# Optimization experiments

Hardware: AMD Instinct MI355X
Metric: run time of the kernel (lower is better)

Reference implementation:

```python
import jax, jax.numpy as jnp
import numpy as np

EPS = 1e-5
NEG_SLOPE = 0.01  # torch F.leaky_relu default


def _batchnorm(h, gamma, beta):
    # BatchNorm1d in training mode: batch stats over node dim, biased variance
    mu = jnp.mean(h, axis=0)
    var = jnp.mean((h - mu) ** 2, axis=0)
    return gamma * (h - mu) * jax.lax.rsqrt(var + EPS) + beta


def setup_inputs() -> dict:
    N, E, H, ED = 16384, 524288, 128, 16
    key = jax.random.key(0)
    ks = jax.random.split(key, 12)
    s = 1.0 / np.sqrt(H)
    return {
        "x": jax.random.normal(ks[0], (N, H), jnp.float32),
        "edge_index": jax.random.randint(ks[1], (2, E), 0, N, jnp.int64),
        "edge_attr": jax.random.normal(ks[2], (E, ED), jnp.float32),
        "Wq": jax.random.normal(ks[3], (H, H), jnp.float32) * s,
        "bq": jnp.zeros((H,), jnp.float32),
        "Wk": jax.random.normal(ks[4], (H, H), jnp.float32) * s,
        "bk": jnp.zeros((H,), jnp.float32),
        "Wv": jax.random.normal(ks[5], (H, H), jnp.float32) * s,
        "bv": jnp.zeros((H,), jnp.float32),
        "We": jax.random.normal(ks[6], (ED, 1), jnp.float32) * (1.0 / np.sqrt(ED)),
        "be": jnp.zeros((1,), jnp.float32),
        "bn1_g": jnp.ones((H,), jnp.float32),
        "bn1_b": jnp.zeros((H,), jnp.float32),
        "W1": jax.random.normal(ks[7], (H, 2 * H), jnp.float32) * s,
        "b1": jnp.zeros((2 * H,), jnp.float32),
        "W2": jax.random.normal(ks[8], (2 * H, H), jnp.float32) * (1.0 / np.sqrt(2 * H)),
        "b2": jnp.zeros((H,), jnp.float32),
        "bn2_g": jnp.ones((H,), jnp.float32),
        "bn2_b": jnp.zeros((H,), jnp.float32),
    }


def reference(x, edge_index, edge_attr, Wq, bq, Wk, bk, Wv, bv, We, be,
              bn1_g, bn1_b, W1, b1, W2, b2, bn2_g, bn2_b):
    N = x.shape[0]
    Q = x @ Wq + bq  # [N, H]
    K = x @ Wk + bk
    V = x @ Wv + bv
    Ebias = (edge_attr @ We + be)[:, 0]  # [E], num_heads == 1
    src, dst = edge_index[0], edge_index[1]
    # per-edge dot product over the FULL hidden dim (as in the source)
    scores = jnp.sum(Q[src] * K[dst], axis=1) + Ebias  # [E]
    scores = jnp.where(scores >= 0, scores, NEG_SLOPE * scores)
    # to_dense_adj scatter-adds edge_attr into a dense [N, N] adjacency
    adj = jnp.zeros((N, N), x.dtype).at[src, dst].add(scores)
    attn = jax.nn.softmax(adj, axis=1)  # dense softmax incl. zero non-edges
    x_new = attn @ V  # [N, H]
    h = _batchnorm(x + x_new, bn1_g, bn1_b)
    ffn = jax.nn.relu(h @ W1 + b1) @ W2 + b2
    return _batchnorm(h + ffn, bn2_g, bn2_b)
```

## Files before the change

kernel.cpp:

```cpp
#include <hip/hip_runtime.h>
#include <hip/hip_bf16.h>
#include <math.h>

#define H 128
#define H2 256
#define SLAB 96
#define LDA 136
#define LDA2 264

typedef __attribute__((ext_vector_type(8))) short s16x8;
typedef __attribute__((ext_vector_type(4))) float f32x4;

__device__ __forceinline__ unsigned short f2bf(float f) {
  unsigned u = __float_as_uint(f);
  unsigned r = (u + 0x7FFFu + ((u >> 16) & 1u)) >> 16;
  return (unsigned short)r;
}
__device__ __forceinline__ float bf2f(unsigned short s) {
  return __uint_as_float(((unsigned)s) << 16);
}

__global__ void wprep(const float* __restrict__ Wq, const float* __restrict__ Wk,
                      const float* __restrict__ Wv, const float* __restrict__ W1,
                      const float* __restrict__ W2,
                      short* qh, short* ql, short* kh, short* kl,
                      short* vh, short* w1h, short* w2h)
{
  int job = blockIdx.z;
  const float* src; short* dh; short* dl = nullptr; int Kd, Nn;
  if (job == 0)      { src = Wq; dh = qh;  dl = ql; Kd = 128; Nn = 128; }
  else if (job == 1) { src = Wk; dh = kh;  dl = kl; Kd = 128; Nn = 128; }
  else if (job == 2) { src = Wv; dh = vh;           Kd = 128; Nn = 128; }
  else if (job == 3) { src = W1; dh = w1h;          Kd = 128; Nn = 256; }
  else               { src = W2; dh = w2h;          Kd = 256; Nn = 128; }
  int t = blockIdx.x * 256 + threadIdx.x;
  if (t >= Kd * Nn) return;
  int n = t / Kd, k = t - n * Kd;
  float v = src[(size_t)k * Nn + n];
  unsigned short h = f2bf(v);
  dh[t] = (short)h;
  if (dl) dl[t] = (short)f2bf(v - bf2f(h));
}

__global__ __launch_bounds__(256) void qkv_mfma(
    const float* __restrict__ x,
    const short* __restrict__ Wqh, const short* __restrict__ Wql,
    const short* __restrict__ Wkh, const short* __restrict__ Wkl,
    const short* __restrict__ Wvh,
    const float* __restrict__ bq, const float* __restrict__ bk,
    const float* __restrict__ bv,
    float* __restrict__ Q, unsigned short* __restrict__ Kbf,
    unsigned short* __restrict__ Vbf, float* __restrict__ SV)
{
  __shared__ __align__(16) short Ahi[64 * LDA];
  __shared__ __align__(16) short Alo[64 * LDA];
  __shared__ __align__(16) short Bhi[128 * LDA];
  __shared__ __align__(16) short Blo[128 * LDA];
  int tid = threadIdx.x;
  int bm = blockIdx.x * 64;
  int wave = tid >> 6, lane = tid & 63;
  int quad = lane >> 4, l16 = lane & 15;
  int wn = wave * 32;

#pragma unroll
  for (int i = 0; i < 4; ++i) {
    int g = i * 256 + tid;
    int row = g >> 4, f = g & 15;
    const float4* xp = (const float4*)&x[(size_t)(bm + row) * H + f * 8];
    float4 v0 = xp[0], v1 = xp[1];
    float vv[8] = {v0.x, v0.y, v0.z, v0.w, v1.x, v1.y, v1.z, v1.w};
    s16x8 hv, lv;
#pragma unroll
    for (int j = 0; j < 8; ++j) {
      unsigned short hh = f2bf(vv[j]);
      hv[j] = (short)hh;
      lv[j] = (short)f2bf(vv[j] - bf2f(hh));
    }
    *(s16x8*)&Ahi[row * LDA + f * 8] = hv;
    *(s16x8*)&Alo[row * LDA + f * 8] = lv;
  }

  for (int ph = 0; ph < 3; ++ph) {
    const short* Bh = (ph == 0) ? Wqh : (ph == 1) ? Wkh : Wvh;
    const short* Bl = (ph == 0) ? Wql : (ph == 1) ? Wkl : nullptr;
    if (ph > 0) __syncthreads();
#pragma unroll
    for (int i = 0; i < 8; ++i) {
      int g = i * 256 + tid;
      int n = g >> 4, f = g & 15;
      *(s16x8*)&Bhi[n * LDA + f * 8] = *(const s16x8*)&Bh[n * H + f * 8];
      if (Bl) *(s16x8*)&Blo[n * LDA + f * 8] = *(const s16x8*)&Bl[n * H + f * 8];
    }
    __syncthreads();

    f32x4 acc[4][2];
#pragma unroll
    for (int mt = 0; mt < 4; ++mt)
#pragma unroll
      for (int nt = 0; nt < 2; ++nt) acc[mt][nt] = (f32x4){0.f, 0.f, 0.f, 0.f};

#pragma unroll
    for (int ks = 0; ks < 4; ++ks) {
      int kof = ks * 32 + quad * 8;
      s16x8 ah[4], al[4], bh[2], bl2[2];
#pragma unroll
      for (int mt = 0; mt < 4; ++mt) {
        ah[mt] = *(s16x8*)&Ahi[(mt * 16 + l16) * LDA + kof];
        al[mt] = *(s16x8*)&Alo[(mt * 16 + l16) * LDA + kof];
      }
#pragma unroll
      for (int nt = 0; nt < 2; ++nt) {
        bh[nt] = *(s16x8*)&Bhi[(wn + nt * 16 + l16) * LDA + kof];
        bl2[nt] = *(s16x8*)&Blo[(wn + nt * 16 + l16) * LDA + kof];
      }
#pragma unroll
      for (int mt = 0; mt < 4; ++mt)
#pragma unroll
        for (int nt = 0; nt < 2; ++nt) {
          acc[mt][nt] = __builtin_amdgcn_mfma_f32_16x16x32_bf16(ah[mt], bh[nt], acc[mt][nt], 0, 0, 0);
          if (ph < 2) {
            acc[mt][nt] = __builtin_amdgcn_mfma_f32_16x16x32_bf16(ah[mt], bl2[nt], acc[mt][nt], 0, 0, 0);
            acc[mt][nt] = __builtin_amdgcn_mfma_f32_16x16x32_bf16(al[mt], bh[nt], acc[mt][nt], 0, 0, 0);
          }
        }
    }

    if (ph == 0) {
#pragma unroll
      for (int nt = 0; nt < 2; ++nt) {
        int col = wn + nt * 16 + l16;
        float bb = bq[col];
#pragma unroll
        for (int mt = 0; mt < 4; ++mt)
#pragma unroll
          for (int r = 0; r < 4; ++r) {
            int row = bm + mt * 16 + quad * 4 + r;
            Q[(size_t)row * H + col] = acc[mt][nt][r] + bb;
          }
      }
    } else if (ph == 1) {
#pragma unroll
      for (int nt = 0; nt < 2; ++nt) {
        int col = wn + nt * 16 + l16;
        float bb = bk[col];
#pragma unroll
        for (int mt = 0; mt < 4; ++mt)
#pragma unroll
          for (int r = 0; r < 4; ++r) {
            int row = bm + mt * 16 + quad * 4 + r;
            Kbf[(size_t)row * H + col] = f2bf(acc[mt][nt][r] + bb);
          }
      }
    } else {
#pragma unroll
      for (int nt = 0; nt < 2; ++nt) {
        int col = wn + nt * 16 + l16;
        float bb = bv[col];
        float ps = 0.f;
#pragma unroll
        for (int mt = 0; mt < 4; ++mt)
#pragma unroll
          for (int r = 0; r < 4; ++r) {
            int row = bm + mt * 16 + quad * 4 + r;
            float v = acc[mt][nt][r] + bb;
            Vbf[(size_t)row * H + col] = f2bf(v);
            ps += v;
          }
        ps += __shfl_xor(ps, 16);
        ps += __shfl_xor(ps, 32);
        if (quad == 0) atomicAdd(&SV[col], ps);
      }
    }
  }
}

__global__ __launch_bounds__(256) void ffn1_mfma(
    const float* __restrict__ h1, const short* __restrict__ W1h,
    const float* __restrict__ b1, const float* __restrict__ A1,
    const float* __restrict__ B1, unsigned short* __restrict__ t1)
{
  __shared__ __align__(16) short As[64 * LDA];
  __shared__ __align__(16) short Bs[256 * LDA];
  int tid = threadIdx.x;
  int bm = blockIdx.x * 64;
  int wave = tid >> 6, lane = tid & 63;
  int quad = lane >> 4, l16 = lane & 15;
  int wn = wave * 64;

#pragma unroll
  for (int i = 0; i < 4; ++i) {
    int g = i * 256 + tid;
    int row = g >> 4, f = g & 15;
    const float4* xp = (const float4*)&h1[(size_t)(bm + row) * H + f * 8];
    float4 v0 = xp[0], v1 = xp[1];
    const float4* ap = (const float4*)&A1[f * 8];
    const float4* bp = (const float4*)&B1[f * 8];
    float4 a0 = ap[0], a1 = ap[1], b0 = bp[0], b1v = bp[1];
    float vv[8] = {a0.x * v0.x + b0.x, a0.y * v0.y + b0.y,
                   a0.z * v0.z + b0.z, a0.w * v0.w + b0.w,
                   a1.x * v1.x + b1v.x, a1.y * v1.y + b1v.y,
                   a1.z * v1.z + b1v.z, a1.w * v1.w + b1v.w};
    s16x8 hv;
#pragma unroll
    for (int j = 0; j < 8; ++j) hv[j] = (short)f2bf(vv[j]);
    *(s16x8*)&As[row * LDA + f * 8] = hv;
  }
#pragma unroll
  for (int i = 0; i < 16; ++i) {
    int g = i * 256 + tid;
    int n = g >> 4, f = g & 15;
    *(s16x8*)&Bs[n * LDA + f * 8] = *(const s16x8*)&W1h[n * H + f * 8];
  }
  __syncthreads();

  f32x4 acc[4][4];
#pragma unroll
  for (int mt = 0; mt < 4; ++mt)
#pragma unroll
    for (int nt = 0; nt < 4; ++nt) acc[mt][nt] = (f32x4){0.f, 0.f, 0.f, 0.f};

#pragma unroll
  for (int ks = 0; ks < 4; ++ks) {
    int kof = ks * 32 + quad * 8;
    s16x8 ah[4], bh[4];
#pragma unroll
    for (int mt = 0; mt < 4; ++mt) ah[mt] = *(s16x8*)&As[(mt * 16 + l16) * LDA + kof];
#pragma unroll
    for (int nt = 0; nt < 4; ++nt) bh[nt] = *(s16x8*)&Bs[(wn + nt * 16 + l16) * LDA + kof];
#pragma unroll
    for (int mt = 0; mt < 4; ++mt)
#pragma unroll
      for (int nt = 0; nt < 4; ++nt)
        acc[mt][nt] = __builtin_amdgcn_mfma_f32_16x16x32_bf16(ah[mt], bh[nt], acc[mt][nt], 0, 0, 0);
  }

#pragma unroll
  for (int nt = 0; nt < 4; ++nt) {
    int col = wn + nt * 16 + l16;
    float bb = b1[col];
#pragma unroll
    for (int mt = 0; mt < 4; ++mt)
#pragma unroll
      for (int r = 0; r < 4; ++r) {
        int row = bm + mt * 16 + quad * 4 + r;
        float v = acc[mt][nt][r] + bb;
        v = v > 0.f ? v : 0.f;
        t1[(size_t)row * H2 + col] = f2bf(v);
      }
  }
}

__global__ __launch_bounds__(256) void ffn2_mfma(
    const unsigned short* __restrict__ t1, const short* __restrict__ W2h,
    const float* __restrict__ b2, const float* __restrict__ h1,
    const float* __restrict__ A1, const float* __restrict__ B1,
    float* __restrict__ h2, float* __restrict__ sum2, float* __restrict__ sq2)
{
  __shared__ __align__(16) short As[64 * LDA2];
  __shared__ __align__(16) short Bs[128 * LDA2];
  int tid = threadIdx.x;
  int bm = blockIdx.x * 64;
  int wave = tid >> 6, lane = tid & 63;
  int quad = lane >> 4, l16 = lane & 15;
  int wn = wave * 32;

#pragma unroll
  for (int i = 0; i < 8; ++i) {
    int g = i * 256 + tid;
    int row = g >> 5, f = g & 31;
    *(s16x8*)&As[row * LDA2 + f * 8] = *(const s16x8*)&t1[(size_t)(bm + row) * H2 + f * 8];
  }
#pragma unroll
  for (int i = 0; i < 16; ++i) {
    int g = i * 256 + tid;
    int n = g >> 5, f = g & 31;
    *(s16x8*)&Bs[n * LDA2 + f * 8] = *(const s16x8*)&W2h[n * H2 + f * 8];
  }
  __syncthreads();

  f32x4 acc[4][2];
#pragma unroll
  for (int mt = 0; mt < 4; ++mt)
#pragma unroll
    for (int nt = 0; nt < 2; ++nt) acc[mt][nt] = (f32x4){0.f, 0.f, 0.f, 0.f};

#pragma unroll
  for (int ks = 0; ks < 8; ++ks) {
    int kof = ks * 32 + quad * 8;
    s16x8 ah[4], bh[2];
#pragma unroll
    for (int mt = 0; mt < 4; ++mt) ah[mt] = *(s16x8*)&As[(mt * 16 + l16) * LDA2 + kof];
#pragma unroll
    for (int nt = 0; nt < 2; ++nt) bh[nt] = *(s16x8*)&Bs[(wn + nt * 16 + l16) * LDA2 + kof];
#pragma unroll
    for (int mt = 0; mt < 4; ++mt)
#pragma unroll
      for (int nt = 0; nt < 2; ++nt)
        acc[mt][nt] = __builtin_amdgcn_mfma_f32_16x16x32_bf16(ah[mt], bh[nt], acc[mt][nt], 0, 0, 0);
  }

#pragma unroll
  for (int nt = 0; nt < 2; ++nt) {
    int col = wn + nt * 16 + l16;
    float bb = b2[col], ra = A1[col], rb = B1[col];
    float ps = 0.f, pq = 0.f;
#pragma unroll
    for (int mt = 0; mt < 4; ++mt)
#pragma unroll
      for (int r = 0; r < 4; ++r) {
        int row = bm + mt * 16 + quad * 4 + r;
        float rr = ra * h1[(size_t)row * H + col] + rb;
        float v = acc[mt][nt][r] + bb + rr;
        h2[(size_t)row * H + col] = v;
        ps += v; pq += v * v;
      }
    ps += __shfl_xor(ps, 16); ps += __shfl_xor(ps, 32);
    pq += __shfl_xor(pq, 16); pq += __shfl_xor(pq, 32);
    if (quad == 0) {
      atomicAdd(&sum2[col], ps);
      atomicAdd(&sq2[col], pq);
    }
  }
}

__global__ void ebfill(const float* __restrict__ ea,
                       const float* __restrict__ We,
                       const float* __restrict__ be,
                       const int* __restrict__ ei,
                       int* __restrict__ cnt,
                       int2* __restrict__ slabDE, int E, int N)
{
  int grp = blockIdx.x & 7;
  int blk = blockIdx.x >> 3;
  int lo = grp * (N >> 3), hi = lo + (N >> 3);
  int per = E >> 8;
  int base = blk * per;
  float4 w0 = *(const float4*)&We[0], w1 = *(const float4*)&We[4];
  float4 w2 = *(const float4*)&We[8], w3 = *(const float4*)&We[12];
  float bias = be[0];
  for (int i = 0; i < per; i += 256) {
    int e = base + i + threadIdx.x;
    if (e >= E) continue;
    int src = ei[e];
    if (src < lo || src >= hi) continue;
    int dst = ei[E + e];
    const float4* p = (const float4*)&ea[(size_t)e * 16];
    float4 a0 = p[0], a1 = p[1], a2 = p[2], a3 = p[3];
    float s = a0.x * w0.x + a0.y * w0.y + a0.z * w0.z + a0.w * w0.w
            + a1.x * w1.x + a1.y * w1.y + a1.z * w1.z + a1.w * w1.w
            + a2.x * w2.x + a2.y * w2.y + a2.z * w2.z + a2.w * w2.w
            + a3.x * w3.x + a3.y * w3.y + a3.z * w3.z + a3.w * w3.w;
    s += bias;
    int pos = atomicAdd(&cnt[src], 1);
    if (pos < SLAB) {
      int2 rec; rec.x = dst; rec.y = __float_as_int(s);
      slabDE[src * SLAB + pos] = rec;
    }
  }
}

__global__ __launch_bounds__(256) void score_slab(
    const float* __restrict__ Q, const unsigned short* __restrict__ Kbf,
    const int* __restrict__ cnt, const int2* __restrict__ slabDE,
    float* __restrict__ sAslab, int N)
{
  int tid = threadIdx.x;
  int team = tid >> 3, sub = tid & 7;
  int local = team & 15;
  int i = blockIdx.x * 2 + (team >> 4);
  int k = cnt[i]; if (k > SLAB) k = SLAB;
  const float4* q4 = (const float4*)(Q + (size_t)i * H);
  float4 qa0 = q4[2 * sub], qa1 = q4[2 * sub + 1];
  float4 qb0 = q4[16 + 2 * sub], qb1 = q4[17 + 2 * sub];
  int base = i * SLAB;

  for (int p = local * 2; p < k; p += 32) {
    int2 de0 = slabDE[base + p];
    bool has1 = (p + 1 < k);
    int2 de1 = has1 ? slabDE[base + p + 1] : de0;
    const s16x8* k0 = (const s16x8*)(Kbf + (size_t)de0.x * H);
    const s16x8* k1 = (const s16x8*)(Kbf + (size_t)de1.x * H);
    s16x8 ka0 = k0[sub], kb0 = k0[8 + sub];
    s16x8 ka1 = k1[sub], kb1 = k1[8 + sub];
    float p0, p1;
    p0 = qa0.x * bf2f((unsigned short)ka0[0]) + qa0.y * bf2f((unsigned short)ka0[1])
       + qa0.z * bf2f((unsigned short)ka0[2]) + qa0.w * bf2f((unsigned short)ka0[3])
       + qa1.x * bf2f((unsigned short)ka0[4]) + qa1.y * bf2f((unsigned short)ka0[5])
       + qa1.z * bf2f((unsigned short)ka0[6]) + qa1.w * bf2f((unsigned short)ka0[7])
       + qb0.x * bf2f((unsigned short)kb0[0]) + qb0.y * bf2f((unsigned short)kb0[1])
       + qb0.z * bf2f((unsigned short)kb0[2]) + qb0.w * bf2f((unsigned short)kb0[3])
       + qb1.x * bf2f((unsigned short)kb0[4]) + qb1.y * bf2f((unsigned short)kb0[5])
       + qb1.z * bf2f((unsigned short)kb0[6]) + qb1.w * bf2f((unsigned short)kb0[7]);
    p1 = qa0.x * bf2f((unsigned short)ka1[0]) + qa0.y * bf2f((unsigned short)ka1[1])
       + qa0.z * bf2f((unsigned short)ka1[2]) + qa0.w * bf2f((unsigned short)ka1[3])
       + qa1.x * bf2f((unsigned short)ka1[4]) + qa1.y * bf2f((unsigned short)ka1[5])
       + qa1.z * bf2f((unsigned short)ka1[6]) + qa1.w * bf2f((unsigned short)ka1[7])
       + qb0.x * bf2f((unsigned short)kb1[0]) + qb0.y * bf2f((unsigned short)kb1[1])
       + qb0.z * bf2f((unsigned short)kb1[2]) + qb0.w * bf2f((unsigned short)kb1[3])
       + qb1.x * bf2f((unsigned short)kb1[4]) + qb1.y * bf2f((unsigned short)kb1[5])
       + qb1.z * bf2f((unsigned short)kb1[6]) + qb1.w * bf2f((unsigned short)kb1[7]);
    p0 += __shfl_xor(p0, 1); p1 += __shfl_xor(p1, 1);
    p0 += __shfl_xor(p0, 2); p1 += __shfl_xor(p1, 2);
    p0 += __shfl_xor(p0, 4); p1 += __shfl_xor(p1, 4);
    if (sub == 0) {
      float s0 = p0 + __int_as_float(de0.y);
      sAslab[base + p] = (s0 >= 0.f) ? s0 : 0.01f * s0;
      if (has1) {
        float s1 = p1 + __int_as_float(de1.y);
        sAslab[base + p + 1] = (s1 >= 0.f) ? s1 : 0.01f * s1;
      }
    }
  }
}

__global__ __launch_bounds__(256) void row_slab(
    const float* __restrict__ x, const unsigned short* __restrict__ Vbf,
    const float* __restrict__ SV, const int* __restrict__ cnt,
    const float* __restrict__ sAslab, const int2* __restrict__ slabDE,
    float* __restrict__ h1, int N)
{
  __shared__ float sv[8][SLAB];
  __shared__ int sd[8][SLAB];
  __shared__ unsigned char sown[8][SLAB];
  int team = threadIdx.x >> 5, lane = threadIdx.x & 31;
  int i = blockIdx.x * 8 + team;
  int k = cnt[i]; if (k > SLAB) k = SLAB;
  int base = i * SLAB;

  for (int p = lane; p < k; p += 32) {
    sv[team][p] = sAslab[base + p];
    sd[team][p] = slabDE[base + p].x;
  }
  __syncthreads();

  for (int p = lane; p < k; p += 32) {
    int d = sd[team][p], o = p;
    for (int q = 0; q < p; ++q)
      if (sd[team][q] == d) { o = q; break; }
    sown[team][p] = (unsigned char)o;
  }
  __syncthreads();
  for (int p = lane; p < k; p += 32)
    if (sown[team][p] != (unsigned char)p)
      atomicAdd(&sv[team][sown[team][p]], sv[team][p]);
  __syncthreads();

  float m = 0.f;
  for (int p = lane; p < k; p += 32)
    if (sown[team][p] == (unsigned char)p) m = fmaxf(m, sv[team][p]);
#pragma unroll
  for (int mask = 16; mask; mask >>= 1) m = fmaxf(m, __shfl_xor(m, mask));
  float em = expf(-m);

  float zl = 0.f;
  for (int p = lane; p < k; p += 32) {
    float cf = 0.f;
    if (sown[team][p] == (unsigned char)p) cf = expf(sv[team][p] - m) - em;
    sv[team][p] = cf;
    zl += cf;
  }
#pragma unroll
  for (int mask = 16; mask; mask >>= 1) zl += __shfl_xor(zl, mask);
  float Zi = 1.f / ((float)N * em + zl);
  __syncthreads();

  const ushort4* V4 = (const ushort4*)Vbf;
  float4 s4 = *(const float4*)&SV[lane * 4];
  float ax = em * s4.x, ay = em * s4.y, az = em * s4.z, aw = em * s4.w;
  int c = 0;
  for (; c + 8 <= k; c += 8) {
    float cf[8]; int dd[8]; ushort4 vv[8];
#pragma unroll
    for (int u = 0; u < 8; ++u) { cf[u] = sv[team][c + u]; dd[u] = sd[team][c + u]; }
#pragma unroll
    for (int u = 0; u < 8; ++u) vv[u] = V4[(size_t)dd[u] * 32 + lane];
#pragma unroll
    for (int u = 0; u < 8; ++u) {
      ax += cf[u] * bf2f(vv[u].x);
      ay += cf[u] * bf2f(vv[u].y);
      az += cf[u] * bf2f(vv[u].z);
      aw += cf[u] * bf2f(vv[u].w);
    }
  }
  for (; c < k; ++c) {
    float cf = sv[team][c];
    ushort4 v0 = V4[(size_t)sd[team][c] * 32 + lane];
    ax += cf * bf2f(v0.x); ay += cf * bf2f(v0.y);
    az += cf * bf2f(v0.z); aw += cf * bf2f(v0.w);
  }
  float4 xx = *(const float4*)&x[(size_t)i * H + lane * 4];
  float4 out;
  out.x = xx.x + ax * Zi; out.y = xx.y + ay * Zi;
  out.z = xx.z + az * Zi; out.w = xx.w + aw * Zi;
  *(float4*)&h1[(size_t)i * H + lane * 4] = out;
}

__global__ __launch_bounds__(128) void colstats(
    const float* __restrict__ X, float* __restrict__ sum,
    float* __restrict__ sumsq, int rowsPerBlock)
{
  int t = threadIdx.x;
  size_t r0 = (size_t)blockIdx.x * rowsPerBlock;
  float s = 0.f, ss = 0.f;
  for (int r = 0; r < rowsPerBlock; ++r) {
    float v = X[(r0 + r) * H + t];
    s += v; ss += v * v;
  }
  atomicAdd(&sum[t], s);
  atomicAdd(&sumsq[t], ss);
}

__global__ void bn_final(const float* __restrict__ sum, const float* __restrict__ sumsq,
                         const float* __restrict__ g, const float* __restrict__ b,
                         float* __restrict__ A, float* __restrict__ B, int n)
{
  int t = threadIdx.x;
  float mu = sum[t] / (float)n;
  float var = sumsq[t] / (float)n - mu * mu;
  float rs = rsqrtf(var + 1e-5f);
  float a = g[t] * rs;
  A[t] = a;
  B[t] = b[t] - a * mu;
}

__global__ void bn_apply(const float* __restrict__ X, const float* __restrict__ A,
                         const float* __restrict__ B, float* __restrict__ Y, size_t n4)
{
  size_t i = (size_t)blockIdx.x * blockDim.x + threadIdx.x;
  if (i >= n4) return;
  float4 v = ((const float4*)X)[i];
  int c = (int)((i * 4) & (H - 1));
  float4 a = *(const float4*)&A[c];
  float4 b = *(const float4*)&B[c];
  v.x = a.x * v.x + b.x; v.y = a.y * v.y + b.y;
  v.z = a.z * v.z + b.z; v.w = a.w * v.w + b.w;
  ((float4*)Y)[i] = v;
}

extern "C" void kernel_launch(void* const* d_in, const int* in_sizes, int n_in,
                              void* d_out, int out_size, void* d_ws, size_t ws_size,
                              hipStream_t stream)
{
  const float* x  = (const float*)d_in[0];
  const int*   ei = (const int*)d_in[1];
  const float* ea = (const float*)d_in[2];
  const float* Wq = (const float*)d_in[3];
  const float* bq = (const float*)d_in[4];
  const float* Wk = (const float*)d_in[5];
  const float* bk = (const float*)d_in[6];
  const float* Wv = (const float*)d_in[7];
  const float* bv = (const float*)d_in[8];
  const float* We = (const float*)d_in[9];
  const float* be = (const float*)d_in[10];
  const float* g1 = (const float*)d_in[11];
  const float* bb1 = (const float*)d_in[12];
  const float* W1 = (const float*)d_in[13];
  const float* b1 = (const float*)d_in[14];
  const float* W2 = (const float*)d_in[15];
  const float* b2 = (const float*)d_in[16];
  const float* g2 = (const float*)d_in[17];
  const float* bb2 = (const float*)d_in[18];

  int N = in_sizes[0] / H;
  int E = in_sizes[2] / 16;
  size_t NH = (size_t)N * H;

  float* Q   = (float*)d_ws;
  float* KmSlot = Q + NH;
  float* h1  = KmSlot + NH;
  unsigned short* Vbf = (unsigned short*)(h1 + NH);
  int2*  slabDE = (int2*)(Vbf + NH);
  float* sAslab = (float*)(slabDE + (size_t)N * SLAB);
  int*   cnt    = (int*)(sAslab + (size_t)N * SLAB);
  float* stats  = (float*)(cnt + N);
  float* SV   = stats;
  float* sum1 = stats + H;
  float* sq1  = stats + 2 * H;
  float* sum2 = stats + 3 * H;
  float* sq2  = stats + 4 * H;
  float* A1   = stats + 5 * H;
  float* B1   = stats + 6 * H;
  float* A2   = stats + 7 * H;
  float* B2   = stats + 8 * H;
  short* wbuf = (short*)(stats + 9 * H + 4);
  short* Wqh = wbuf;
  short* Wql = Wqh + 16384;
  short* Wkh = Wql + 16384;
  short* Wkl = Wkh + 16384;
  short* Wvh = Wkl + 16384;
  short* W1h = Wvh + 16384;
  short* W2h = W1h + 32768;
  unsigned short* Kbf = (unsigned short*)KmSlot;
  unsigned short* t1 = (unsigned short*)Q;
  float* h2 = KmSlot;

  hipMemsetAsync(cnt, 0, (size_t)N * sizeof(int), stream);
  hipMemsetAsync(stats, 0, (size_t)5 * H * sizeof(float), stream);

  wprep<<<dim3(128, 1, 5), 256, 0, stream>>>(Wq, Wk, Wv, W1, W2,
      Wqh, Wql, Wkh, Wkl, Wvh, W1h, W2h);

  qkv_mfma<<<dim3(N / 64), 256, 0, stream>>>(
      x, Wqh, Wql, Wkh, Wkl, Wvh, bq, bk, bv, Q, Kbf, Vbf, SV);

  ebfill<<<dim3(2048), 256, 0, stream>>>(ea, We, be, ei, cnt, slabDE, E, N);
  score_slab<<<dim3(N / 2), 256, 0, stream>>>(Q, Kbf, cnt, slabDE, sAslab, N);
  row_slab<<<dim3(N / 8), 256, 0, stream>>>(x, Vbf, SV, cnt, sAslab, slabDE, h1, N);

  colstats<<<dim3(128), 128, 0, stream>>>(h1, sum1, sq1, N / 128);
  bn_final<<<dim3(1), H, 0, stream>>>(sum1, sq1, g1, bb1, A1, B1, N);

  ffn1_mfma<<<dim3(N / 64), 256, 0, stream>>>(h1, W1h, b1, A1, B1, t1);
  ffn2_mfma<<<dim3(N / 64), 256, 0, stream>>>(t1, W2h, b2, h1, A1, B1, h2, sum2, sq2);

  bn_final<<<dim3(1), H, 0, stream>>>(sum2, sq2, g2, bb2, A2, B2, N);
  bn_apply<<<dim3((int)((NH / 4 + 255) / 256)), 256, 0, stream>>>(h2, A2, B2, (float*)d_out, NH / 4);
}
```

Measured before the change: 264.9 us.

## Load MFMA weight fragments directly into registers and fold BN finalize into consumers

The QKV, FFN1 and FFN2 GEMM kernels stop staging weight tiles in shared memory and instead load each wave's B fragments straight from global memory into registers. This removes large LDS allocations and the associated stores and barriers, which can raise occupancy. The two single-block bn_final launches are removed, and each consumer kernel recomputes the BatchNorm scale and shift from the sum and sum-of-squares buffers. The trade-off is more register pressure, redundant global weight reads per wave that now rely on cache hits, and repeated rsqrt work in every thread.

```diff
diff --git a/kernel.cpp b/kernel.cpp
--- a/kernel.cpp
+++ b/kernel.cpp
@@ -7,6 +7,7 @@
 #define SLAB 96
 #define LDA 136
 #define LDA2 264
+#define EPS 1e-5f
 
 typedef __attribute__((ext_vector_type(8))) short s16x8;
 typedef __attribute__((ext_vector_type(4))) float f32x4;
@@ -54,8 +55,6 @@
 {
   __shared__ __align__(16) short Ahi[64 * LDA];
   __shared__ __align__(16) short Alo[64 * LDA];
-  __shared__ __align__(16) short Bhi[128 * LDA];
-  __shared__ __align__(16) short Blo[128 * LDA];
   int tid = threadIdx.x;
   int bm = blockIdx.x * 64;
   int wave = tid >> 6, lane = tid & 63;
@@ -79,19 +78,25 @@
     *(s16x8*)&Ahi[row * LDA + f * 8] = hv;
     *(s16x8*)&Alo[row * LDA + f * 8] = lv;
   }
+  __syncthreads();
 
   for (int ph = 0; ph < 3; ++ph) {
     const short* Bh = (ph == 0) ? Wqh : (ph == 1) ? Wkh : Wvh;
     const short* Bl = (ph == 0) ? Wql : (ph == 1) ? Wkl : nullptr;
-    if (ph > 0) __syncthreads();
-#pragma unroll
-    for (int i = 0; i < 8; ++i) {
-      int g = i * 256 + tid;
-      int n = g >> 4, f = g & 15;
-      *(s16x8*)&Bhi[n * LDA + f * 8] = *(const s16x8*)&Bh[n * H + f * 8];
-      if (Bl) *(s16x8*)&Blo[n * LDA + f * 8] = *(const s16x8*)&Bl[n * H + f * 8];
-    }
-    __syncthreads();
+
+    s16x8 bh[2][4], bl2[2][4];
+#pragma unroll
+    for (int nt = 0; nt < 2; ++nt)
+#pragma unroll
+      for (int ks = 0; ks < 4; ++ks)
+        bh[nt][ks] = *(const s16x8*)&Bh[(size_t)(wn + nt * 16 + l16) * H + ks * 32 + quad * 8];
+    if (Bl) {
+#pragma unroll
+      for (int nt = 0; nt < 2; ++nt)
+#pragma unroll
+        for (int ks = 0; ks < 4; ++ks)
+          bl2[nt][ks] = *(const s16x8*)&Bl[(size_t)(wn + nt * 16 + l16) * H + ks * 32 + quad * 8];
+    }
 
     f32x4 acc[4][2];
 #pragma unroll
@@ -102,25 +107,20 @@
 #pragma unroll
     for (int ks = 0; ks < 4; ++ks) {
       int kof = ks * 32 + quad * 8;
-      s16x8 ah[4], al[4], bh[2], bl2[2];
+      s16x8 ah[4], al[4];
 #pragma unroll
       for (int mt = 0; mt < 4; ++mt) {
         ah[mt] = *(s16x8*)&Ahi[(mt * 16 + l16) * LDA + kof];
         al[mt] = *(s16x8*)&Alo[(mt * 16 + l16) * LDA + kof];
       }
 #pragma unroll
-      for (int nt = 0; nt < 2; ++nt) {
-        bh[nt] = *(s16x8*)&Bhi[(wn + nt * 16 + l16) * LDA + kof];
-        bl2[nt] = *(s16x8*)&Blo[(wn + nt * 16 + l16) * LDA + kof];
-      }
-#pragma unroll
       for (int mt = 0; mt < 4; ++mt)
 #pragma unroll
         for (int nt = 0; nt < 2; ++nt) {
-          acc[mt][nt] = __builtin_amdgcn_mfma_f32_16x16x32_bf16(ah[mt], bh[nt], acc[mt][nt], 0, 0, 0);
+          acc[mt][nt] = __builtin_amdgcn_mfma_f32_16x16x32_bf16(ah[mt], bh[nt][ks], acc[mt][nt], 0, 0, 0);
           if (ph < 2) {
-            acc[mt][nt] = __builtin_amdgcn_mfma_f32_16x16x32_bf16(ah[mt], bl2[nt], acc[mt][nt], 0, 0, 0);
-            acc[mt][nt] = __builtin_amdgcn_mfma_f32_16x16x32_bf16(al[mt], bh[nt], acc[mt][nt], 0, 0, 0);
+            acc[mt][nt] = __builtin_amdgcn_mfma_f32_16x16x32_bf16(ah[mt], bl2[nt][ks], acc[mt][nt], 0, 0, 0);
+            acc[mt][nt] = __builtin_amdgcn_mfma_f32_16x16x32_bf16(al[mt], bh[nt][ks], acc[mt][nt], 0, 0, 0);
           }
         }
     }
@@ -176,41 +176,50 @@
 
 __global__ __launch_bounds__(256) void ffn1_mfma(
     const float* __restrict__ h1, const short* __restrict__ W1h,
-    const float* __restrict__ b1, const float* __restrict__ A1,
-    const float* __restrict__ B1, unsigned short* __restrict__ t1)
+    const float* __restrict__ b1,
+    const float* __restrict__ sum1, const float* __restrict__ sq1,
+    const float* __restrict__ g1, const float* __restrict__ bb1,
+    unsigned short* __restrict__ t1, float invN)
 {
   __shared__ __align__(16) short As[64 * LDA];
-  __shared__ __align__(16) short Bs[256 * LDA];
   int tid = threadIdx.x;
   int bm = blockIdx.x * 64;
   int wave = tid >> 6, lane = tid & 63;
   int quad = lane >> 4, l16 = lane & 15;
   int wn = wave * 64;
 
+  int f = tid & 15;
+  float aP[8], bP[8];
+#pragma unroll
+  for (int j = 0; j < 8; ++j) {
+    int c = f * 8 + j;
+    float mu = sum1[c] * invN;
+    float var = sq1[c] * invN - mu * mu;
+    float rs = rsqrtf(var + EPS);
+    float a = g1[c] * rs;
+    aP[j] = a;
+    bP[j] = bb1[c] - a * mu;
+  }
+
 #pragma unroll
   for (int i = 0; i < 4; ++i) {
     int g = i * 256 + tid;
-    int row = g >> 4, f = g & 15;
+    int row = g >> 4;
     const float4* xp = (const float4*)&h1[(size_t)(bm + row) * H + f * 8];
     float4 v0 = xp[0], v1 = xp[1];
-    const float4* ap = (const float4*)&A1[f * 8];
-    const float4* bp = (const float4*)&B1[f * 8];
-    float4 a0 = ap[0], a1 = ap[1], b0 = bp[0], b1v = bp[1];
-    float vv[8] = {a0.x * v0.x + b0.x, a0.y * v0.y + b0.y,
-                   a0.z * v0.z + b0.z, a0.w * v0.w + b0.w,
-                   a1.x * v1.x + b1v.x, a1.y * v1.y + b1v.y,
-                   a1.z * v1.z + b1v.z, a1.w * v1.w + b1v.w};
+    float vv[8] = {v0.x, v0.y, v0.z, v0.w, v1.x, v1.y, v1.z, v1.w};
     s16x8 hv;
 #pragma unroll
-    for (int j = 0; j < 8; ++j) hv[j] = (short)f2bf(vv[j]);
+    for (int j = 0; j < 8; ++j) hv[j] = (short)f2bf(aP[j] * vv[j] + bP[j]);
     *(s16x8*)&As[row * LDA + f * 8] = hv;
   }
-#pragma unroll
-  for (int i = 0; i < 16; ++i) {
-    int g = i * 256 + tid;
-    int n = g >> 4, f = g & 15;
-    *(s16x8*)&Bs[n * LDA + f * 8] = *(const s16x8*)&W1h[n * H + f * 8];
-  }
+
+  s16x8 bh[4][4];
+#pragma unroll
+  for (int nt = 0; nt < 4; ++nt)
+#pragma unroll
+    for (int ks = 0; ks < 4; ++ks)
+      bh[nt][ks] = *(const s16x8*)&W1h[(size_t)(wn + nt * 16 + l16) * H + ks * 32 + quad * 8];
   __syncthreads();
 
   f32x4 acc[4][4];
@@ -222,16 +231,14 @@
 #pragma unroll
   for (int ks = 0; ks < 4; ++ks) {
     int kof = ks * 32 + quad * 8;
-    s16x8 ah[4], bh[4];
+    s16x8 ah[4];
 #pragma unroll
     for (int mt = 0; mt < 4; ++mt) ah[mt] = *(s16x8*)&As[(mt * 16 + l16) * LDA + kof];
 #pragma unroll
-    for (int nt = 0; nt < 4; ++nt) bh[nt] = *(s16x8*)&Bs[(wn + nt * 16 + l16) * LDA + kof];
-#pragma unroll
     for (int mt = 0; mt < 4; ++mt)
 #pragma unroll
       for (int nt = 0; nt < 4; ++nt)
-        acc[mt][nt] = __builtin_amdgcn_mfma_f32_16x16x32_bf16(ah[mt], bh[nt], acc[mt][nt], 0, 0, 0);
+        acc[mt][nt] = __builtin_amdgcn_mfma_f32_16x16x32_bf16(ah[mt], bh[nt][ks], acc[mt][nt], 0, 0, 0);
   }
 
 #pragma unroll
@@ -253,11 +260,12 @@
 __global__ __launch_bounds__(256) void ffn2_mfma(
     const unsigned short* __restrict__ t1, const short* __restrict__ W2h,
     const float* __restrict__ b2, const float* __restrict__ h1,
-    const float* __restrict__ A1, const float* __restrict__ B1,
-    float* __restrict__ h2, float* __restrict__ sum2, float* __restrict__ sq2)
+    const float* __restrict__ sum1, const float* __restrict__ sq1,
+    const float* __restrict__ g1, const float* __restrict__ bb1,
+    float* __restrict__ h2, float* __restrict__ sum2, float* __restrict__ sq2,
+    float invN)
 {
   __shared__ __align__(16) short As[64 * LDA2];
-  __shared__ __align__(16) short Bs[128 * LDA2];
   int tid = threadIdx.x;
   int bm = blockIdx.x * 64;
   int wave = tid >> 6, lane = tid & 63;
@@ -270,12 +278,13 @@
     int row = g >> 5, f = g & 31;
     *(s16x8*)&As[row * LDA2 + f * 8] = *(const s16x8*)&t1[(size_t)(bm + row) * H2 + f * 8];
   }
-#pragma unroll
-  for (int i = 0; i < 16; ++i) {
-    int g = i * 256 + tid;
-    int n = g >> 5, f = g & 31;
-    *(s16x8*)&Bs[n * LDA2 + f * 8] = *(const s16x8*)&W2h[n * H2 + f * 8];
-  }
+
+  s16x8 bh[2][8];
+#pragma unroll
+  for (int nt = 0; nt < 2; ++nt)
+#pragma unroll
+    for (int ks = 0; ks < 8; ++ks)
+      bh[nt][ks] = *(const s16x8*)&W2h[(size_t)(wn + nt * 16 + l16) * H2 + ks * 32 + quad * 8];
   __syncthreads();
 
   f32x4 acc[4][2];
@@ -287,22 +296,25 @@
 #pragma unroll
   for (int ks = 0; ks < 8; ++ks) {
     int kof = ks * 32 + quad * 8;
-    s16x8 ah[4], bh[2];
+    s16x8 ah[4];
 #pragma unroll
     for (int mt = 0; mt < 4; ++mt) ah[mt] = *(s16x8*)&As[(mt * 16 + l16) * LDA2 + kof];
 #pragma unroll
-    for (int nt = 0; nt < 2; ++nt) bh[nt] = *(s16x8*)&Bs[(wn + nt * 16 + l16) * LDA2 + kof];
-#pragma unroll
     for (int mt = 0; mt < 4; ++mt)
 #pragma unroll
       for (int nt = 0; nt < 2; ++nt)
-        acc[mt][nt] = __builtin_amdgcn_mfma_f32_16x16x32_bf16(ah[mt], bh[nt], acc[mt][nt], 0, 0, 0);
+        acc[mt][nt] = __builtin_amdgcn_mfma_f32_16x16x32_bf16(ah[mt], bh[nt][ks], acc[mt][nt], 0, 0, 0);
   }
 
 #pragma unroll
   for (int nt = 0; nt < 2; ++nt) {
     int col = wn + nt * 16 + l16;
-    float bb = b2[col], ra = A1[col], rb = B1[col];
+    float mu = sum1[col] * invN;
+    float var = sq1[col] * invN - mu * mu;
+    float rs = rsqrtf(var + EPS);
+    float ra = g1[col] * rs;
+    float rb = bb1[col] - ra * mu;
+    float bb = b2[col];
     float ps = 0.f, pq = 0.f;
 #pragma unroll
     for (int mt = 0; mt < 4; ++mt)
@@ -510,30 +522,28 @@
   atomicAdd(&sumsq[t], ss);
 }
 
-__global__ void bn_final(const float* __restrict__ sum, const float* __restrict__ sumsq,
-                         const float* __restrict__ g, const float* __restrict__ b,
-                         float* __restrict__ A, float* __restrict__ B, int n)
-{
-  int t = threadIdx.x;
-  float mu = sum[t] / (float)n;
-  float var = sumsq[t] / (float)n - mu * mu;
-  float rs = rsqrtf(var + 1e-5f);
-  float a = g[t] * rs;
-  A[t] = a;
-  B[t] = b[t] - a * mu;
-}
-
-__global__ void bn_apply(const float* __restrict__ X, const float* __restrict__ A,
-                         const float* __restrict__ B, float* __restrict__ Y, size_t n4)
+__global__ void bn_apply(const float* __restrict__ X,
+                         const float* __restrict__ sum2, const float* __restrict__ sq2,
+                         const float* __restrict__ g2, const float* __restrict__ bb2,
+                         float* __restrict__ Y, size_t n4, float invN)
 {
   size_t i = (size_t)blockIdx.x * blockDim.x + threadIdx.x;
   if (i >= n4) return;
   float4 v = ((const float4*)X)[i];
   int c = (int)((i * 4) & (H - 1));
-  float4 a = *(const float4*)&A[c];
-  float4 b = *(const float4*)&B[c];
-  v.x = a.x * v.x + b.x; v.y = a.y * v.y + b.y;
-  v.z = a.z * v.z + b.z; v.w = a.w * v.w + b.w;
+  float4 s = *(const float4*)&sum2[c];
+  float4 q = *(const float4*)&sq2[c];
+  float4 g = *(const float4*)&g2[c];
+  float4 b = *(const float4*)&bb2[c];
+  float mu, var, rs, a;
+  mu = s.x * invN; var = q.x * invN - mu * mu; rs = rsqrtf(var + EPS);
+  a = g.x * rs; v.x = a * v.x + (b.x - a * mu);
+  mu = s.y * invN; var = q.y * invN - mu * mu; rs = rsqrtf(var + EPS);
+  a = g.y * rs; v.y = a * v.y + (b.y - a * mu);
+  mu = s.z * invN; var = q.z * invN - mu * mu; rs = rsqrtf(var + EPS);
+  a = g.z * rs; v.z = a * v.z + (b.z - a * mu);
+  mu = s.w * invN; var = q.w * invN - mu * mu; rs = rsqrtf(var + EPS);
+  a = g.w * rs; v.w = a * v.w + (b.w - a * mu);
   ((float4*)Y)[i] = v;
 }
 
@@ -564,6 +574,7 @@
   int N = in_sizes[0] / H;
   int E = in_sizes[2] / 16;
   size_t NH = (size_t)N * H;
+  float invN = 1.0f / (float)N;
 
   float* Q   = (float*)d_ws;
   float* KmSlot = Q + NH;
@@ -578,10 +589,6 @@
   float* sq1  = stats + 2 * H;
   float* sum2 = stats + 3 * H;
   float* sq2  = stats + 4 * H;
-  float* A1   = stats + 5 * H;
-  float* B1   = stats + 6 * H;
-  float* A2   = stats + 7 * H;
-  float* B2   = stats + 8 * H;
   short* wbuf = (short*)(stats + 9 * H + 4);
   short* Wqh = wbuf;
   short* Wql = Wqh + 16384;
@@ -608,11 +615,11 @@
   row_slab<<<dim3(N / 8), 256, 0, stream>>>(x, Vbf, SV, cnt, sAslab, slabDE, h1, N);
 
   colstats<<<dim3(128), 128, 0, stream>>>(h1, sum1, sq1, N / 128);
-  bn_final<<<dim3(1), H, 0, stream>>>(sum1, sq1, g1, bb1, A1, B1, N);
-
-  ffn1_mfma<<<dim3(N / 64), 256, 0, stream>>>(h1, W1h, b1, A1, B1, t1);
-  ffn2_mfma<<<dim3(N / 64), 256, 0, stream>>>(t1, W2h, b2, h1, A1, B1, h2, sum2, sq2);
-
-  bn_final<<<dim3(1), H, 0, stream>>>(sum2, sq2, g2, bb2, A2, B2, N);
-  bn_apply<<<dim3((int)((NH / 4 + 255) / 256)), 256, 0, stream>>>(h2, A2, B2, (float*)d_out, NH / 4);
-}
+
+  ffn1_mfma<<<dim3(N / 64), 256, 0, stream>>>(h1, W1h, b1, sum1, sq1, g1, bb1, t1, invN);
+  ffn2_mfma<<<dim3(N / 64), 256, 0, stream>>>(t1, W2h, b2, h1, sum1, sq1, g1, bb1,
+                                              h2, sum2, sq2, invN);
+
+  bn_apply<<<dim3((int)((NH / 4 + 255) / 256)), 256, 0, stream>>>(
+      h2, sum2, sq2, g2, bb2, (float*)d_out, NH / 4, invN);
+}
```

Result: no change. 262.6 us (-0.9%).
